# Optimization experiments

Hardware: AMD Instinct MI355X
Metric: run time of the kernel (lower is better)

## Reference

```python
import jax, jax.numpy as jnp
import numpy as np

DIM = 768
HEADS = 8
DHEAD = 64
DEMB = HEADS * DHEAD  # 512
EPS = 1e-5


def layer_norm(x, g, b):
    mu = jnp.mean(x, axis=-1, keepdims=True)
    var = jnp.var(x, axis=-1, keepdims=True)
    return (x - mu) * jax.lax.rsqrt(var + EPS) * g + b


def setup_inputs() -> dict:
    key = jax.random.key(0)
    ks = jax.random.split(key, 9)
    b, t, n_src, n_ltn = 2, 4, 8192, 64
    inv = 1.0 / np.sqrt(DIM)
    return {
        "src": jax.random.normal(ks[0], (b, t, n_src, DIM), jnp.float32),
        "ltn": jax.random.normal(ks[1], (b, t, n_ltn, DIM), jnp.float32),
        "g_src": jnp.ones((DIM,), jnp.float32),
        "b_src": jnp.zeros((DIM,), jnp.float32),
        "g_ltn": jnp.ones((DIM,), jnp.float32),
        "b_ltn": jnp.zeros((DIM,), jnp.float32),
        # weights stored (in, out) so y = x @ W  (== torch Linear with W.T)
        "Wq": jax.random.normal(ks[2], (DIM, DEMB), jnp.float32) * inv,
        "Wkv": jax.random.normal(ks[3], (DIM, 2 * DEMB), jnp.float32) * inv,
        "Wo": jax.random.normal(ks[4], (DEMB, DIM), jnp.float32) * (1.0 / np.sqrt(DEMB)),
    }


def reference(src, ltn, g_src, b_src, g_ltn, b_ltn, Wq, Wkv, Wo):
    b, t, n_ltn, _ = ltn.shape
    n_src = src.shape[2]
    scale = DHEAD ** -0.5

    src_n = layer_norm(src, g_src, b_src)
    ltn_n = layer_norm(ltn, g_ltn, b_ltn)

    q = ltn_n @ Wq                                  # [b,t,nl,DEMB]
    ctx = jnp.concatenate([src_n, ltn_n], axis=-2)  # [b,t,ns+nl,DIM]
    kv = ctx @ Wkv                                  # [b,t,ns+nl,2*DEMB]
    k, v = jnp.split(kv, 2, axis=-1)

    def to_heads(x):  # b t n (h d) -> b h t n d
        B, T, N, _ = x.shape
        return x.reshape(B, T, N, HEADS, DHEAD).transpose(0, 3, 1, 2, 4)

    q, k, v = to_heads(q), to_heads(k), to_heads(v)

    attn = jnp.einsum('bhtid,bhtjd->bhtij', q, k) * scale
    attn = jax.nn.softmax(attn - jax.lax.stop_gradient(attn.max(axis=-1, keepdims=True)), axis=-1)
    out = jnp.einsum('bhtij,bhtjd->bhtid', attn, v)  # [b,h,t,nl,d]

    out = out.transpose(0, 2, 3, 1, 4).reshape(b, t, n_ltn, DEMB)
    return out @ Wo
```

## Files before the change

### kernel.cpp

```cpp
#include <hip/hip_runtime.h>
#include <hip/hip_bf16.h>
#include <type_traits>


#define N_SRC 8192
#define N_LTN 64
#define N_CTX 8256
#define NBT 8
#define MROWS 66048
#define DIMK 768
#define DEMB 512
#define NSPLIT 16
#define NTILES 65

typedef short short8 __attribute__((ext_vector_type(8)));
typedef float floatx4 __attribute__((ext_vector_type(4)));
typedef __attribute__((address_space(1))) void gvoid;
typedef __attribute__((address_space(3))) void lvoid;

__device__ inline ushort f2bf(float f) {
    union { float f; unsigned u; } v; v.f = f;
    unsigned u = v.u;
    return (ushort)((u + 0x7fffu + ((u >> 16) & 1u)) >> 16);
}

__global__ __launch_bounds__(256) void transpose_all(
        const float* __restrict__ Wkv, const float* __restrict__ Wq,
        const float* __restrict__ Wo, ushort* __restrict__ WkvT,
        ushort* __restrict__ WqT, ushort* __restrict__ WoT) {
    __shared__ ushort tile[64][65];
    int z = blockIdx.z;
    const float* in; ushort* out; int R, C;
    if (z == 0)      { in = Wkv; out = WkvT; R = 768; C = 1024; }
    else if (z == 1) { in = Wq;  out = WqT;  R = 768; C = 512;  }
    else             { in = Wo;  out = WoT;  R = 512; C = 768;  }
    int C0 = blockIdx.x * 64, R0 = blockIdx.y * 64;
    if (C0 >= C || R0 >= R) return;
    int tc = threadIdx.x & 63, tr4 = threadIdx.x >> 6;
#pragma unroll
    for (int j = 0; j < 16; j++) {
        int r = tr4 + j * 4;
        tile[r][tc] = f2bf(in[(size_t)(R0 + r) * C + C0 + tc]);
    }
    __syncthreads();
#pragma unroll
    for (int j = 0; j < 16; j++) {
        int c = tr4 + j * 4;
        out[(size_t)(C0 + c) * R + R0 + tc] = tile[tc][c];
    }
}

__global__ __launch_bounds__(256) void ln_kernel(
        const float* __restrict__ src, const float* __restrict__ ltn,
        const float* __restrict__ gs, const float* __restrict__ bs,
        const float* __restrict__ gl, const float* __restrict__ bl,
        ushort* __restrict__ ctx, ushort* __restrict__ qin) {
    int r = blockIdx.x * 4 + (threadIdx.x >> 6);
    int lane = threadIdx.x & 63;
    int bt = r / N_CTX;
    int i = r - bt * N_CTX;
    const float *x, *g, *b;
    int isl = (i >= N_SRC);
    if (!isl) { x = src + ((size_t)bt * N_SRC + i) * DIMK; g = gs; b = bs; }
    else      { x = ltn + ((size_t)bt * N_LTN + (i - N_SRC)) * DIMK; g = gl; b = bl; }
    float4 v[3]; float s = 0.f, s2 = 0.f;
#pragma unroll
    for (int t = 0; t < 3; t++) {
        float4 xv = *(const float4*)(x + t * 256 + lane * 4);
        v[t] = xv;
        s  += xv.x + xv.y + xv.z + xv.w;
        s2 += xv.x * xv.x + xv.y * xv.y + xv.z * xv.z + xv.w * xv.w;
    }
#pragma unroll
    for (int off = 32; off >= 1; off >>= 1) {
        s  += __shfl_xor(s,  off, 64);
        s2 += __shfl_xor(s2, off, 64);
    }
    float mu  = s * (1.0f / 768.0f);
    float var = s2 * (1.0f / 768.0f) - mu * mu;
    float rs  = rsqrtf(var + 1e-5f);
    ushort* crow = ctx + (size_t)r * DIMK;
    ushort* qrow = isl ? (qin + (size_t)(bt * N_LTN + (i - N_SRC)) * DIMK) : nullptr;
#pragma unroll
    for (int t = 0; t < 3; t++) {
        int idx = t * 256 + lane * 4;
        float4 gv = *(const float4*)(g + idx);
        float4 bv = *(const float4*)(b + idx);
        ushort4 u;
        u.x = f2bf((v[t].x - mu) * rs * gv.x + bv.x);
        u.y = f2bf((v[t].y - mu) * rs * gv.y + bv.y);
        u.z = f2bf((v[t].z - mu) * rs * gv.z + bv.z);
        u.w = f2bf((v[t].w - mu) * rs * gv.w + bv.w);
        *(ushort4*)(crow + idx) = u;
        if (isl) *(ushort4*)(qrow + idx) = u;
    }
}

template <typename CT>
__global__ __launch_bounds__(256) void gemm_bt(
        const ushort* __restrict__ A, const ushort* __restrict__ B,
        CT* __restrict__ C, int M, int N, int K) {
    __shared__ ushort lA[128 * 64];
    __shared__ ushort lB[128 * 64];
    int tid = threadIdx.x;
    int lane = tid & 63, wave = tid >> 6;
    int wm = wave >> 1, wn = wave & 1;
    int bn = blockIdx.x, bm = blockIdx.y;

    floatx4 acc[4][4];
#pragma unroll
    for (int mi = 0; mi < 4; mi++)
#pragma unroll
        for (int ni = 0; ni < 4; ni++) acc[mi][ni] = (floatx4){0.f, 0.f, 0.f, 0.f};

    int srow = lane >> 3;
    int schunk = (lane & 7) ^ srow;
    int quad = lane >> 4, lr = lane & 15;
    const int kiters = K >> 6;

    for (int kt = 0; kt < kiters; kt++) {
#pragma unroll
        for (int c2 = 0; c2 < 4; c2++) {
            int row = c2 * 32 + wave * 8 + srow;
            const ushort* gpA = A + ((size_t)(bm * 128 + row) * K + kt * 64 + schunk * 8);
            ushort* lpA = lA + (c2 * 32 + wave * 8) * 64 + lane * 8;
            __builtin_amdgcn_global_load_lds((gvoid*)gpA, (lvoid*)lpA, 16, 0, 0);
            const ushort* gpB = B + ((size_t)(bn * 128 + row) * K + kt * 64 + schunk * 8);
            ushort* lpB = lB + (c2 * 32 + wave * 8) * 64 + lane * 8;
            __builtin_amdgcn_global_load_lds((gvoid*)gpB, (lvoid*)lpB, 16, 0, 0);
        }
        __syncthreads();
#pragma unroll
        for (int ks = 0; ks < 2; ks++) {
            short8 av[4], bv[4];
            int slot = ((ks * 4 + quad) ^ (lane & 7)) * 8;
#pragma unroll
            for (int mi = 0; mi < 4; mi++)
                av[mi] = *(const short8*)(lA + (wm * 64 + mi * 16 + lr) * 64 + slot);
#pragma unroll
            for (int ni = 0; ni < 4; ni++)
                bv[ni] = *(const short8*)(lB + (wn * 64 + ni * 16 + lr) * 64 + slot);
#pragma unroll
            for (int mi = 0; mi < 4; mi++)
#pragma unroll
                for (int ni = 0; ni < 4; ni++)
                    acc[mi][ni] = __builtin_amdgcn_mfma_f32_16x16x32_bf16(
                        av[mi], bv[ni], acc[mi][ni], 0, 0, 0);
        }
        __syncthreads();
    }
#pragma unroll
    for (int mi = 0; mi < 4; mi++)
#pragma unroll
        for (int ni = 0; ni < 4; ni++)
#pragma unroll
            for (int r = 0; r < 4; r++) {
                int row = bm * 128 + wm * 64 + mi * 16 + quad * 4 + r;
                int col = bn * 128 + wn * 64 + ni * 16 + lr;
                float vv = acc[mi][ni][r];
                if constexpr (std::is_same<CT, ushort>::value)
                    C[(size_t)row * N + col] = f2bf(vv);
                else
                    C[(size_t)row * N + col] = vv;
            }
}

#define PR 136

__global__ __launch_bounds__(256) void attn_flash(
        const float* __restrict__ qf, const ushort* __restrict__ kvb,
        float* __restrict__ Op, float* __restrict__ ml) {
    __shared__ ushort lK[128 * 64];
    __shared__ ushort lVT[64 * PR];
    __shared__ ushort lP[64 * PR];

    int comb = blockIdx.x, split = blockIdx.y;
    int bt = comb >> 3, h = comb & 7;
    int tid = threadIdx.x;
    int w = tid >> 6, lane = tid & 63, quad = lane >> 4, lr = lane & 15;

    const ushort* kptr = kvb + (size_t)bt * N_CTX * 1024 + h * 64;
    const ushort* vptr = kptr + 512;

    short8 qa[2];
    {
        const float* p0 = qf + (size_t)(bt * 64 + w * 16 + lr) * DEMB + h * 64;
#pragma unroll
        for (int kc = 0; kc < 2; kc++) {
            const float* p = p0 + kc * 32 + quad * 8;
            float4 f0 = *(const float4*)p;
            float4 f1 = *(const float4*)(p + 4);
            short8 v;
            v[0] = f2bf(f0.x); v[1] = f2bf(f0.y); v[2] = f2bf(f0.z); v[3] = f2bf(f0.w);
            v[4] = f2bf(f1.x); v[5] = f2bf(f1.y); v[6] = f2bf(f1.z); v[7] = f2bf(f1.w);
            qa[kc] = v;
        }
    }

    floatx4 accO[4];
#pragma unroll
    for (int nt = 0; nt < 4; nt++) accO[nt] = (floatx4){0.f, 0.f, 0.f, 0.f};
    float m_run[4], l_run[4];
#pragma unroll
    for (int r = 0; r < 4; r++) { m_run[r] = -1e30f; l_run[r] = 0.f; }

    for (int t = split; t < NTILES; t += NSPLIT) {
        int kbase = t * 128;
        __syncthreads();

#pragma unroll
        for (int c2 = 0; c2 < 4; c2++) {
            int jloc = w * 32 + c2 * 8 + (lane >> 3);
            int chunk = (lane & 7) ^ ((lane >> 3) & 7);
            int jg = kbase + jloc; if (jg > N_CTX - 1) jg = N_CTX - 1;
            const ushort* gp = kptr + (size_t)jg * 1024 + chunk * 8;
            ushort* lp = lK + (w * 32 + c2 * 8) * 64 + lane * 8;
            __builtin_amdgcn_global_load_lds((gvoid*)gp, (lvoid*)lp, 16, 0, 0);
        }

        {
            int k0 = kbase + lane * 2;
            bool valid = (k0 + 1) < N_CTX;
            int k0c = valid ? k0 : (N_CTX - 2);
            const ushort* r0 = vptr + (size_t)k0c * 1024 + w * 16;
            const ushort* r1 = r0 + 1024;
            uint4 a0 = *(const uint4*)r0;
            uint4 a1 = *(const uint4*)(r0 + 8);
            uint4 b0 = *(const uint4*)r1;
            uint4 b1 = *(const uint4*)(r1 + 8);
            if (!valid) {
                a0 = make_uint4(0, 0, 0, 0); a1 = a0; b0 = a0; b1 = a0;
            }
            unsigned av8[8] = {a0.x, a0.y, a0.z, a0.w, a1.x, a1.y, a1.z, a1.w};
            unsigned bv8[8] = {b0.x, b0.y, b0.z, b0.w, b1.x, b1.y, b1.z, b1.w};
#pragma unroll
            for (int i = 0; i < 8; i++) {
                unsigned la = av8[i] & 0xffffu, ha = av8[i] >> 16;
                unsigned lb = bv8[i] & 0xffffu, hb = bv8[i] >> 16;
                *(unsigned*)(lVT + (w * 16 + 2 * i) * PR + lane * 2)     = la | (lb << 16);
                *(unsigned*)(lVT + (w * 16 + 2 * i + 1) * PR + lane * 2) = ha | (hb << 16);
            }
        }
        __syncthreads();

        floatx4 accS[8];
#pragma unroll
        for (int nt = 0; nt < 8; nt++) accS[nt] = (floatx4){0.f, 0.f, 0.f, 0.f};
#pragma unroll
        for (int kc = 0; kc < 2; kc++) {
#pragma unroll
            for (int nt = 0; nt < 8; nt++) {
                int kr = nt * 16 + lr;
                int slot = (kc * 4 + quad) ^ (kr & 7);
                short8 bv = *(const short8*)(lK + kr * 64 + slot * 8);
                accS[nt] = __builtin_amdgcn_mfma_f32_16x16x32_bf16(
                    qa[kc], bv, accS[nt], 0, 0, 0);
            }
        }

        float sc[8][4];
        float tmax[4] = {-1e30f, -1e30f, -1e30f, -1e30f};
#pragma unroll
        for (int nt = 0; nt < 8; nt++) {
            bool vk = (kbase + nt * 16 + lr) < N_CTX;
#pragma unroll
            for (int r = 0; r < 4; r++) {
                float s = vk ? accS[nt][r] * 0.125f : -1e30f;
                sc[nt][r] = s;
                tmax[r] = fmaxf(tmax[r], s);
            }
        }
#pragma unroll
        for (int r = 0; r < 4; r++) {
#pragma unroll
            for (int d = 1; d < 16; d <<= 1) tmax[r] = fmaxf(tmax[r], __shfl_xor(tmax[r], d, 64));
        }
        float alpha[4], lsum[4];
#pragma unroll
        for (int r = 0; r < 4; r++) {
            float mn = fmaxf(m_run[r], tmax[r]);
            alpha[r] = __expf(m_run[r] - mn);
            m_run[r] = mn;
            lsum[r] = 0.f;
        }

#pragma unroll
        for (int nt = 0; nt < 8; nt++) {
#pragma unroll
            for (int r = 0; r < 4; r++) {
                float p = __expf(sc[nt][r] - m_run[r]);
                lsum[r] += p;
                lP[(w * 16 + quad * 4 + r) * PR + nt * 16 + lr] = f2bf(p);
            }
        }
#pragma unroll
        for (int r = 0; r < 4; r++) {
#pragma unroll
            for (int d = 1; d < 16; d <<= 1) lsum[r] += __shfl_xor(lsum[r], d, 64);
            l_run[r] = l_run[r] * alpha[r] + lsum[r];
        }
#pragma unroll
        for (int nt = 0; nt < 4; nt++) {
            accO[nt][0] *= alpha[0]; accO[nt][1] *= alpha[1];
            accO[nt][2] *= alpha[2]; accO[nt][3] *= alpha[3];
        }

        short8 av[4];
#pragma unroll
        for (int kc = 0; kc < 4; kc++)
            av[kc] = *(const short8*)(lP + (w * 16 + lr) * PR + kc * 32 + quad * 8);
#pragma unroll
        for (int nt = 0; nt < 4; nt++)
#pragma unroll
            for (int kc = 0; kc < 4; kc++) {
                short8 bv = *(const short8*)(lVT + (nt * 16 + lr) * PR + kc * 32 + quad * 8);
                accO[nt] = __builtin_amdgcn_mfma_f32_16x16x32_bf16(av[kc], bv, accO[nt], 0, 0, 0);
            }
    }

    float* opb = Op + (size_t)(comb * NSPLIT + split) * 64 * 64;
#pragma unroll
    for (int nt = 0; nt < 4; nt++)
#pragma unroll
        for (int r = 0; r < 4; r++)
            opb[(w * 16 + quad * 4 + r) * 64 + nt * 16 + lr] = accO[nt][r];
    if (lr == 0) {
#pragma unroll
        for (int r = 0; r < 4; r++) {
            int row = w * 16 + quad * 4 + r;
            float* mlp = ml + ((size_t)(comb * NSPLIT + split) * 64 + row) * 2;
            mlp[0] = m_run[r]; mlp[1] = l_run[r];
        }
    }
}

__global__ __launch_bounds__(64) void attn_combine(
        const float* __restrict__ Op, const float* __restrict__ ml,
        ushort* __restrict__ outp) {
    int bx = blockIdx.x;
    int comb = bx >> 6, q = bx & 63;
    int bt = comb >> 3, h = comb & 7;
    int d = threadIdx.x;
    float M = -1e30f;
    for (int s = 0; s < NSPLIT; s++)
        M = fmaxf(M, ml[((size_t)(comb * NSPLIT + s) * 64 + q) * 2]);
    float L = 0.f, O = 0.f;
    for (int s = 0; s < NSPLIT; s++) {
        const float* p = ml + ((size_t)(comb * NSPLIT + s) * 64 + q) * 2;
        float wgt = __expf(p[0] - M);
        L = fmaf(wgt, p[1], L);
        O = fmaf(wgt, Op[((size_t)(comb * NSPLIT + s) * 64 + q) * 64 + d], O);
    }
    outp[(size_t)(bt * 64 + q) * DEMB + h * 64 + d] = f2bf(O / L);
}

extern "C" void kernel_launch(void* const* d_in, const int* in_sizes, int n_in,
                              void* d_out, int out_size, void* d_ws, size_t ws_size,
                              hipStream_t stream) {
    const float* src   = (const float*)d_in[0];
    const float* ltn   = (const float*)d_in[1];
    const float* g_src = (const float*)d_in[2];
    const float* b_src = (const float*)d_in[3];
    const float* g_ltn = (const float*)d_in[4];
    const float* b_ltn = (const float*)d_in[5];
    const float* Wq    = (const float*)d_in[6];
    const float* Wkv   = (const float*)d_in[7];
    const float* Wo    = (const float*)d_in[8];
    float* out = (float*)d_out;

    char* ws = (char*)d_ws;
    size_t off = 0;
    auto alloc = [&](size_t bytes) -> void* {
        void* p = ws + off;
        off += (bytes + 255) & ~(size_t)255;
        return p;
    };
    ushort* ctx  = (ushort*)alloc((size_t)MROWS * DIMK * 2);
    ushort* qin  = (ushort*)alloc((size_t)512 * DIMK * 2);
    ushort* WkvT = (ushort*)alloc((size_t)1024 * DIMK * 2);
    ushort* WqT  = (ushort*)alloc((size_t)512 * DIMK * 2);
    ushort* WoT  = (ushort*)alloc((size_t)768 * DEMB * 2);
    ushort* kvb  = (ushort*)alloc((size_t)MROWS * 1024 * 2);
    float*  qf   = (float*) alloc((size_t)512 * DEMB * 4);
    ushort* outp = (ushort*)alloc((size_t)512 * DEMB * 2);

    float* Op  = (float*)(void*)ctx;
    float* mlb = Op + (size_t)64 * NSPLIT * 64 * 64;

    transpose_all<<<dim3(16, 12, 3), 256, 0, stream>>>(Wkv, Wq, Wo, WkvT, WqT, WoT);

    ln_kernel<<<MROWS / 4, 256, 0, stream>>>(src, ltn, g_src, b_src, g_ltn, b_ltn, ctx, qin);

    gemm_bt<ushort><<<dim3(1024 / 128, MROWS / 128), 256, 0, stream>>>(
        ctx, WkvT, kvb, MROWS, 1024, DIMK);
    gemm_bt<float><<<dim3(512 / 128, 512 / 128), 256, 0, stream>>>(
        qin, WqT, qf, 512, 512, DIMK);

    attn_flash<<<dim3(64, NSPLIT), 256, 0, stream>>>(qf, kvb, Op, mlb);
    attn_combine<<<4096, 64, 0, stream>>>(Op, mlb, outp);

    gemm_bt<float><<<dim3(768 / 128, 512 / 128), 256, 0, stream>>>(
        outp, WoT, out, 512, 768, DEMB);
}
```

Baseline: 531.2 us.

## Widen KV projection GEMM tile to 128x256 and halve attention splits

Adds a gemm_bt2 kernel that computes 128x256 output tiles per block, with each wave holding a 64x128 accumulator. It is used for the large ctx@Wkv projection, so the A tiles are reused across twice as many output columns and fewer blocks reload the activation rows. The attention split count also drops from 16 to 8, which shrinks the partial-output buffers and the combine work but gives the flash kernel fewer blocks. The wider tile doubles the accumulator registers and enlarges LDS use, which may lower occupancy.

```diff
diff --git a/kernel.cpp b/kernel.cpp
--- a/kernel.cpp
+++ b/kernel.cpp
@@ -10,7 +10,7 @@
 #define MROWS 66048
 #define DIMK 768
 #define DEMB 512
-#define NSPLIT 16
+#define NSPLIT 8
 #define NTILES 65
 
 typedef short short8 __attribute__((ext_vector_type(8)));
@@ -157,6 +157,79 @@
             for (int r = 0; r < 4; r++) {
                 int row = bm * 128 + wm * 64 + mi * 16 + quad * 4 + r;
                 int col = bn * 128 + wn * 64 + ni * 16 + lr;
+                float vv = acc[mi][ni][r];
+                if constexpr (std::is_same<CT, ushort>::value)
+                    C[(size_t)row * N + col] = f2bf(vv);
+                else
+                    C[(size_t)row * N + col] = vv;
+            }
+}
+
+template <typename CT>
+__global__ __launch_bounds__(256) void gemm_bt2(
+        const ushort* __restrict__ A, const ushort* __restrict__ B,
+        CT* __restrict__ C, int M, int N, int K) {
+    __shared__ ushort lA[128 * 64];
+    __shared__ ushort lB[256 * 64];
+    int tid = threadIdx.x;
+    int lane = tid & 63, wave = tid >> 6;
+    int wm = wave >> 1, wn = wave & 1;
+    int bn = blockIdx.x, bm = blockIdx.y;
+
+    floatx4 acc[4][8];
+#pragma unroll
+    for (int mi = 0; mi < 4; mi++)
+#pragma unroll
+        for (int ni = 0; ni < 8; ni++) acc[mi][ni] = (floatx4){0.f, 0.f, 0.f, 0.f};
+
+    int srow = lane >> 3;
+    int schunk = (lane & 7) ^ srow;
+    int quad = lane >> 4, lr = lane & 15;
+    const int kiters = K >> 6;
+
+    for (int kt = 0; kt < kiters; kt++) {
+#pragma unroll
+        for (int c2 = 0; c2 < 12; c2++) {
+            int row = c2 * 32 + wave * 8 + srow;
+            if (c2 < 4) {
+                const ushort* gp = A + ((size_t)(bm * 128 + row) * K + kt * 64 + schunk * 8);
+                ushort* lp = lA + (c2 * 32 + wave * 8) * 64 + lane * 8;
+                __builtin_amdgcn_global_load_lds((gvoid*)gp, (lvoid*)lp, 16, 0, 0);
+            } else {
+                int brow = row - 128;
+                const ushort* gp = B + ((size_t)(bn * 256 + brow) * K + kt * 64 + schunk * 8);
+                ushort* lp = lB + ((c2 - 4) * 32 + wave * 8) * 64 + lane * 8;
+                __builtin_amdgcn_global_load_lds((gvoid*)gp, (lvoid*)lp, 16, 0, 0);
+            }
+        }
+        __syncthreads();
+#pragma unroll
+        for (int ks = 0; ks < 2; ks++) {
+            int slot = ((ks * 4 + quad) ^ (lane & 7)) * 8;
+            short8 av[4], bv[8];
+#pragma unroll
+            for (int mi = 0; mi < 4; mi++)
+                av[mi] = *(const short8*)(lA + (wm * 64 + mi * 16 + lr) * 64 + slot);
+#pragma unroll
+            for (int ni = 0; ni < 8; ni++)
+                bv[ni] = *(const short8*)(lB + (wn * 128 + ni * 16 + lr) * 64 + slot);
+#pragma unroll
+            for (int mi = 0; mi < 4; mi++)
+#pragma unroll
+                for (int ni = 0; ni < 8; ni++)
+                    acc[mi][ni] = __builtin_amdgcn_mfma_f32_16x16x32_bf16(
+                        av[mi], bv[ni], acc[mi][ni], 0, 0, 0);
+        }
+        __syncthreads();
+    }
+#pragma unroll
+    for (int mi = 0; mi < 4; mi++)
+#pragma unroll
+        for (int ni = 0; ni < 8; ni++)
+#pragma unroll
+            for (int r = 0; r < 4; r++) {
+                int row = bm * 128 + wm * 64 + mi * 16 + quad * 4 + r;
+                int col = bn * 256 + wn * 128 + ni * 16 + lr;
                 float vv = acc[mi][ni][r];
                 if constexpr (std::is_same<CT, ushort>::value)
                     C[(size_t)row * N + col] = f2bf(vv);
@@ -391,7 +464,7 @@
 
     ln_kernel<<<MROWS / 4, 256, 0, stream>>>(src, ltn, g_src, b_src, g_ltn, b_ltn, ctx, qin);
 
-    gemm_bt<ushort><<<dim3(1024 / 128, MROWS / 128), 256, 0, stream>>>(
+    gemm_bt2<ushort><<<dim3(1024 / 256, MROWS / 128), 256, 0, stream>>>(
         ctx, WkvT, kvb, MROWS, 1024, DIMK);
     gemm_bt<float><<<dim3(512 / 128, 512 / 128), 256, 0, stream>>>(
         qin, WqT, qf, 512, 512, DIMK);
```

Result: slower. 614.2 us (+15.6%).
